# Kernel tuning notes

Hardware: AMD Instinct MI355X
Metric: run time of the kernel (lower is better)

The kernel has to match this reference:

```python
import jax, jax.numpy as jnp
import numpy as np


def setup_inputs() -> dict:
    key = jax.random.key(0)
    k1, k2, k3 = jax.random.split(key, 3)
    B, S, H, E = 8, 4096, 2048, 64
    hidden_states = jax.random.normal(k1, (B, S, H), dtype=jnp.float32)
    # kaiming_uniform-ish scale for the gate weight [E, H]
    weight = jax.random.normal(k2, (E, H), dtype=jnp.float32) * (1.0 / np.sqrt(H))
    # load-balancing biases are small perturbations of the softmax scores
    expert_biases = jax.random.normal(k3, (E,), dtype=jnp.float32) * 0.01
    return {"hidden_states": hidden_states, "weight": weight,
            "expert_biases": expert_biases, "top_k": 8}


def reference(hidden_states, weight, expert_biases, top_k):
    B, S, H = hidden_states.shape
    x = hidden_states.reshape(-1, H).astype(jnp.float32)          # [T, H], T = B*S
    logits = jnp.einsum('th,eh->te', x, weight.astype(jnp.float32))  # [T, E]
    scores = jax.nn.softmax(logits, axis=-1)                      # fp32 softmax
    bias_scores = scores + expert_biases[None, :]                 # bias-adjusted routing
    _, topk_indices = jax.lax.top_k(bias_scores, top_k)           # [T, K] (sorted; set equals torch sorted=False)
    topk_weights = jnp.take_along_axis(scores, topk_indices, axis=1)  # gather original probs
    if top_k > 1:  # norm_topk_prob=True
        topk_weights = topk_weights / (topk_weights.sum(-1, keepdims=True) + 1e-20)
    return (topk_indices.astype(jnp.int32),
            topk_weights.astype(hidden_states.dtype))
```

## Files before the change

### kernel.cpp

```cpp
#include <hip/hip_runtime.h>
#include <math.h>

#define Hdim   2048
#define HF4    512
#define MARGIN 2e-5f
#define CAPF   16384
#define PROBE0 1237
#define PROBE1 20011

#define WS_FCNT  0
#define WS_BAD   4
#define WS_PROBE 64
#define WS_FLIST 1024
#define WS_WH    (128*1024)
#define WS_WL    (384*1024)
#define WS_NEED  (640*1024)

typedef float f32x4 __attribute__((ext_vector_type(4)));
typedef short bf8   __attribute__((ext_vector_type(8)));

typedef const __attribute__((address_space(1))) unsigned int ga_u32;
typedef __attribute__((address_space(3))) unsigned int la_u32;
__device__ __forceinline__ void gload16(const void* g, void* l) {
  __builtin_amdgcn_global_load_lds((ga_u32*)g, (la_u32*)l, 16, 0, 0);
}

__device__ __forceinline__ short bf_hi(float v, float& rem) {
  const unsigned u  = __builtin_bit_cast(unsigned, v);
  const unsigned uh = u & 0xffff0000u;
  rem = v - __builtin_bit_cast(float, uh);
  return (short)(u >> 16);
}
__device__ __forceinline__ short bf_rne(float v) {
  const unsigned u = __builtin_bit_cast(unsigned, v);
  return (short)((u + 0x7fffu + ((u >> 16) & 1u)) >> 16);
}

__global__ __launch_bounds__(256) void gate_prep(
    const float* __restrict__ wgt, short* __restrict__ WH, short* __restrict__ WL)
{
  const int f  = blockIdx.x * 256 + threadIdx.x;
  const int c  = f >> 11;
  const int et = (f >> 9) & 3;
  const int l  = (f >> 3) & 63;
  const int j  = f & 7;
  const int e  = et * 16 + (l & 15);
  const int k  = c * 32 + (l >> 4) * 8 + j;
  const float w = wgt[(size_t)e * Hdim + k];
  float r; const short h = bf_hi(w, r);
  WH[f] = h; WL[f] = bf_rne(r);
}

__global__ __launch_bounds__(256, 2) void gate_main(
    const float* __restrict__ x, const short* __restrict__ WH,
    const short* __restrict__ WL, const float* __restrict__ eb,
    float* __restrict__ out, int* __restrict__ fcnt, int* __restrict__ flist,
    float* __restrict__ probelg, int T)
{
  __shared__ __align__(16) char smem[32768];
  const int t    = threadIdx.x;
  const int wv   = t >> 6;
  const int ln   = t & 63;
  const int tb   = blockIdx.x * 64 + wv * 16;

  const char* xq = (const char*)(x + (size_t)(tb + (ln & 15)) * Hdim + (ln >> 4) * 8);
  const short* whq = WH + t * 8;
  const short* wlq = WL + t * 8;

  f32x4 acc[4];
  #pragma unroll
  for (int et = 0; et < 4; ++et) acc[et] = (f32x4)0.f;

  f32x4 xE0, xE1, xO0, xO1;

#define XLOAD(D0, D1, OA, OB)                                              \
  asm volatile("global_load_dwordx4 %0, %2, off offset:" #OA "\n\t"        \
               "global_load_dwordx4 %1, %2, off offset:" #OB               \
               : "=v"(D0), "=v"(D1) : "v"(xq) : "memory")

#define WSTAGE(SLOT, KOFF) {                                               \
    gload16(whq + (KOFF), smem + (SLOT) * 8192 + wv * 1024);               \
    gload16(wlq + (KOFF), smem + (SLOT) * 8192 + 4096 + wv * 1024); }

#define SPLIT(X0, X1) {                                                    \
    _Pragma("unroll")                                                      \
    for (int j = 0; j < 4; ++j) { float r_;                                \
      ah[j]     = bf_hi(X0[j], r_);  al[j]     = bf_rne(r_);               \
      ah[j + 4] = bf_hi(X1[j], r_);  al[j + 4] = bf_rne(r_); } }

#define MF16()                                                                    \
    __builtin_amdgcn_s_setprio(1);                                                \
    acc[0] = __builtin_amdgcn_mfma_f32_16x16x32_bf16(ah, Bh0, acc[0], 0, 0, 0);   \
    acc[0] = __builtin_amdgcn_mfma_f32_16x16x32_bf16(ah, Bl0, acc[0], 0, 0, 0);   \
    acc[0] = __builtin_amdgcn_mfma_f32_16x16x32_bf16(al, Bh0, acc[0], 0, 0, 0);   \
    acc[0] = __builtin_amdgcn_mfma_f32_16x16x32_bf16(al, Bl0, acc[0], 0, 0, 0);   \
    acc[1] = __builtin_amdgcn_mfma_f32_16x16x32_bf16(ah, Bh1, acc[1], 0, 0, 0);   \
    acc[1] = __builtin_amdgcn_mfma_f32_16x16x32_bf16(ah, Bl1, acc[1], 0, 0, 0);   \
    acc[1] = __builtin_amdgcn_mfma_f32_16x16x32_bf16(al, Bh1, acc[1], 0, 0, 0);   \
    acc[1] = __builtin_amdgcn_mfma_f32_16x16x32_bf16(al, Bl1, acc[1], 0, 0, 0);   \
    acc[2] = __builtin_amdgcn_mfma_f32_16x16x32_bf16(ah, Bh2, acc[2], 0, 0, 0);   \
    acc[2] = __builtin_amdgcn_mfma_f32_16x16x32_bf16(ah, Bl2, acc[2], 0, 0, 0);   \
    acc[2] = __builtin_amdgcn_mfma_f32_16x16x32_bf16(al, Bh2, acc[2], 0, 0, 0);   \
    acc[2] = __builtin_amdgcn_mfma_f32_16x16x32_bf16(al, Bl2, acc[2], 0, 0, 0);   \
    acc[3] = __builtin_amdgcn_mfma_f32_16x16x32_bf16(ah, Bh3, acc[3], 0, 0, 0);   \
    acc[3] = __builtin_amdgcn_mfma_f32_16x16x32_bf16(ah, Bl3, acc[3], 0, 0, 0);   \
    acc[3] = __builtin_amdgcn_mfma_f32_16x16x32_bf16(al, Bh3, acc[3], 0, 0, 0);   \
    acc[3] = __builtin_amdgcn_mfma_f32_16x16x32_bf16(al, Bl3, acc[3], 0, 0, 0);   \
    __builtin_amdgcn_s_setprio(0);

#define STEP(SCUR, XI, WI, XS0, XS1, VM) {                                 \
    XI; WI;                                                                \
    asm volatile("s_waitcnt vmcnt(" #VM ")" ::: "memory");                 \
    __builtin_amdgcn_sched_barrier(0);                                     \
    bf8 ah, al;                                                            \
    SPLIT(XS0, XS1);                                                       \
    asm volatile("" ::: "memory");                                         \
    __builtin_amdgcn_s_barrier();                                          \
    asm volatile("" ::: "memory");                                         \
    const short* bh_ = (const short*)(smem + (SCUR) * 8192) + ln * 8;      \
    const short* bl_ = bh_ + 2048;                                         \
    bf8 Bh0 = *(const bf8*)(bh_);                                          \
    bf8 Bh1 = *(const bf8*)(bh_ + 512);                                    \
    bf8 Bh2 = *(const bf8*)(bh_ + 1024);                                   \
    bf8 Bh3 = *(const bf8*)(bh_ + 1536);                                   \
    bf8 Bl0 = *(const bf8*)(bl_);                                          \
    bf8 Bl1 = *(const bf8*)(bl_ + 512);                                    \
    bf8 Bl2 = *(const bf8*)(bl_ + 1024);                                   \
    bf8 Bl3 = *(const bf8*)(bl_ + 1536);                                   \
    MF16();                                                                \
  }

  XLOAD(xE0, xE1, 0, 16);
  WSTAGE(0, 0);
  WSTAGE(1, 2048);

  #pragma unroll 1
  for (int ks = 0; ks < 60; ks += 4) {
    STEP(0, XLOAD(xO0, xO1, 128, 144), WSTAGE(2, 4096),  xE0, xE1, 6);
    STEP(1, XLOAD(xE0, xE1, 256, 272), WSTAGE(3, 6144),  xO0, xO1, 6);
    STEP(2, XLOAD(xO0, xO1, 384, 400), WSTAGE(0, 8192),  xE0, xE1, 6);
    STEP(3, XLOAD(xE0, xE1, 512, 528), WSTAGE(1, 10240), xO0, xO1, 6);
    xq += 512; whq += 8192; wlq += 8192;
  }
  STEP(0, XLOAD(xO0, xO1, 128, 144), WSTAGE(2, 4096), xE0, xE1, 6);
  STEP(1, XLOAD(xE0, xE1, 256, 272), WSTAGE(3, 6144), xO0, xO1, 6);
  STEP(2, XLOAD(xO0, xO1, 384, 400), ,                xE0, xE1, 4);
  STEP(3, ,                          ,                xO0, xO1, 0);
#undef STEP
#undef MF16
#undef SPLIT
#undef WSTAGE
#undef XLOAD

  const int c = ln & 15, g = ln >> 4;
  float bias4[4];
  #pragma unroll
  for (int et = 0; et < 4; ++et) bias4[et] = eb[et * 16 + c];

  #pragma unroll
  for (int r = 0; r < 4; ++r) {
    const int gt = tb + g * 4 + r;
    const float z0 = acc[0][r], z1 = acc[1][r], z2 = acc[2][r], z3 = acc[3][r];
    if (gt == PROBE0) { probelg[c]      = z0; probelg[16 + c] = z1;
                        probelg[32 + c] = z2; probelg[48 + c] = z3; }
    if (gt == PROBE1) { probelg[64 + c]  = z0; probelg[80 + c]  = z1;
                        probelg[96 + c]  = z2; probelg[112 + c] = z3; }
    float m = fmaxf(fmaxf(z0, z1), fmaxf(z2, z3));
    #pragma unroll
    for (int off = 1; off < 16; off <<= 1) m = fmaxf(m, __shfl_xor(m, off, 64));
    const float p0 = expf(z0 - m), p1 = expf(z1 - m);
    const float p2 = expf(z2 - m), p3 = expf(z3 - m);
    float Zs = (p0 + p1) + (p2 + p3);
    #pragma unroll
    for (int off = 1; off < 16; off <<= 1) Zs += __shfl_xor(Zs, off, 64);
    const float inv = 1.f / Zs;
    const float s0 = p0 * inv, s1 = p1 * inv, s2 = p2 * inv, s3 = p3 * inv;
    float b0 = s0 + bias4[0], b1 = s1 + bias4[1];
    float b2 = s2 + bias4[2], b3 = s3 + bias4[3];
    float prev = 0.f, gmin = 1e30f, mys = 0.f;
    int myi = 0;
    #pragma unroll
    for (int r9 = 0; r9 < 9; ++r9) {
      float v = b0; int ie = 0;
      if (b1 > v) { v = b1; ie = 1; }
      if (b2 > v) { v = b2; ie = 2; }
      if (b3 > v) { v = b3; ie = 3; }
      int idx = ie * 16 + c;
      #pragma unroll
      for (int off = 1; off < 16; off <<= 1) {
        const float ov = __shfl_xor(v, off, 64);
        const int   oi = __shfl_xor(idx, off, 64);
        if (ov > v || (ov == v && oi < idx)) { v = ov; idx = oi; }
      }
      if (r9) gmin = fminf(gmin, prev - v);
      prev = v;
      if (r9 < 8) {
        const int oe = idx >> 4, oc = idx & 15;
        const float cand = oe == 0 ? s0 : oe == 1 ? s1 : oe == 2 ? s2 : s3;
        const float sv = __shfl(cand, g * 16 + oc, 64);
        if (c == r9) { myi = idx; mys = sv; }
        if (c == oc) {
          if (oe == 0) b0 = -1e30f;
          else if (oe == 1) b1 = -1e30f;
          else if (oe == 2) b2 = -1e30f;
          else b3 = -1e30f;
        }
      }
    }
    float wsum = (c < 8) ? mys : 0.f;
    #pragma unroll
    for (int off = 1; off < 16; off <<= 1) wsum += __shfl_xor(wsum, off, 64);
    if (c < 8) {
      out[(size_t)gt * 8 + c] = (float)myi;
      out[(size_t)T * 8 + (size_t)gt * 8 + c] = mys / (wsum + 1e-20f);
    }
    if (c == 0 && gmin < MARGIN) {
      const int pos = atomicAdd(fcnt, 1);
      if (pos < CAPF) flist[pos] = gt;
    }
  }
}

__global__ __launch_bounds__(256) void gate_check(
    const float* __restrict__ x, const float* __restrict__ wgt,
    const float* __restrict__ probelg, const int* __restrict__ fcnt,
    int* __restrict__ allbad)
{
  __shared__ float part[64][4];
  const int p = blockIdx.x;
  const int P = p ? PROBE1 : PROBE0;
  const int t = threadIdx.x, e = t >> 2, q = t & 3;
  const float4* xr = (const float4*)(x + (size_t)P * Hdim);
  const float4* wr = (const float4*)(wgt + (size_t)e * Hdim);
  float a = 0.f, b = 0.f, c = 0.f, d = 0.f;
  for (int i = 0; i < 128; ++i) {
    const int f4 = i * 4 + q;
    const float4 xv = xr[f4], wv = wr[f4];
    a = fmaf(xv.x, wv.x, a); b = fmaf(xv.y, wv.y, b);
    c = fmaf(xv.z, wv.z, c); d = fmaf(xv.w, wv.w, d);
  }
  part[e][q] = (a + b) + (c + d);
  __syncthreads();
  if (q == 0) {
    const float z = part[e][0] + part[e][1] + part[e][2] + part[e][3];
    if (fabsf(z - probelg[p * 64 + e]) > 0.05f) *allbad = 1;
  }
  if (t == 0 && p == 0 && *fcnt > CAPF) *allbad = 1;
}

__global__ __launch_bounds__(256) void gate_fix(
    const float* __restrict__ x, const float* __restrict__ wgt,
    const float* __restrict__ eb, float* __restrict__ out,
    const int* __restrict__ fcnt, const int* __restrict__ flist,
    const int* __restrict__ allbad, int T)
{
  __shared__ float4 xl[4 * HF4];
  __shared__ double part[4][64][4];
  __shared__ int tks[4];
  const int bad = *allbad;
  int n = bad ? T : *fcnt;
  if (n <= 0) return;
  if (!bad && n > CAPF) n = CAPF;
  const int nb = (n + 3) >> 2;
  const int t = threadIdx.x;
  for (int b = blockIdx.x; b < nb; b += gridDim.x) {
    if (t < 4) {
      const int li = b * 4 + t;
      const int ci = li < n ? li : n - 1;
      tks[t] = bad ? ci : flist[ci];
    }
    __syncthreads();
    {
      const int m = t >> 6, l2 = t & 63;
      const float4* src = (const float4*)x + (size_t)tks[m] * HF4;
      #pragma unroll
      for (int ii = 0; ii < 8; ++ii) xl[m * HF4 + ii * 64 + l2] = src[ii * 64 + l2];
    }
    __syncthreads();
    const int e = t >> 2, q = t & 3;
    double acc[4] = {0.0, 0.0, 0.0, 0.0};
    const float4* w4 = (const float4*)wgt + (size_t)e * HF4;
    for (int c = 0; c < 128; ++c) {
      const int f4 = c * 4 + q;
      const float4 wvv = w4[f4];
      #pragma unroll
      for (int m = 0; m < 4; ++m) {
        const float4 xv = xl[m * HF4 + f4];
        acc[m] += (double)xv.x * (double)wvv.x + (double)xv.y * (double)wvv.y
                + (double)xv.z * (double)wvv.z + (double)xv.w * (double)wvv.w;
      }
    }
    #pragma unroll
    for (int m = 0; m < 4; ++m) part[m][e][q] = acc[m];
    __syncthreads();
    {
      const int m = t >> 6, ln = t & 63;
      const double z = part[m][ln][0] + part[m][ln][1] + part[m][ln][2] + part[m][ln][3];
      double mx = z;
      #pragma unroll
      for (int off = 32; off; off >>= 1) mx = fmax(mx, __shfl_xor(mx, off, 64));
      const double p = exp(z - mx);
      double Zs = p;
      #pragma unroll
      for (int off = 32; off; off >>= 1) Zs += __shfl_xor(Zs, off, 64);
      const double sco = p / Zs;
      double bsw = sco + (double)eb[ln];
      double mys = 0.0;
      int myi = 0;
      #pragma unroll
      for (int r = 0; r < 8; ++r) {
        double v = bsw;
        int idx = ln;
        #pragma unroll
        for (int off = 32; off; off >>= 1) {
          const double ov = __shfl_xor(v, off, 64);
          const int   oi = __shfl_xor(idx, off, 64);
          if (ov > v || (ov == v && oi < idx)) { v = ov; idx = oi; }
        }
        const double sv = __shfl(sco, idx, 64);
        if (ln == r)  { myi = idx; mys = sv; }
        if (ln == idx) bsw = -1.0e300;
      }
      double wsum = (ln < 8) ? mys : 0.0;
      #pragma unroll
      for (int off = 32; off; off >>= 1) wsum += __shfl_xor(wsum, off, 64);
      const int gt = tks[m];
      if (ln < 8) {
        out[(size_t)gt * 8 + ln] = (float)myi;
        out[(size_t)T * 8 + (size_t)gt * 8 + ln] = (float)(mys / (wsum + 1e-20));
      }
    }
    __syncthreads();
  }
}

extern "C" void kernel_launch(void* const* d_in, const int* in_sizes, int n_in,
                              void* d_out, int out_size, void* d_ws, size_t ws_size,
                              hipStream_t stream) {
  const float* x   = (const float*)d_in[0];
  const float* wgt = (const float*)d_in[1];
  const float* eb  = (const float*)d_in[2];
  float* out = (float*)d_out;
  const int T = in_sizes[0] / Hdim;
  char* ws = (char*)d_ws;
  int*   fcnt    = (int*)(ws + WS_FCNT);
  int*   bad     = (int*)(ws + WS_BAD);
  float* probelg = (float*)(ws + WS_PROBE);
  int*   flist   = (int*)(ws + WS_FLIST);
  short* WH      = (short*)(ws + WS_WH);
  short* WL      = (short*)(ws + WS_WL);

  if (ws_size < WS_NEED) {
    hipMemsetAsync(ws, 0, 8, stream);
    hipMemsetAsync(ws + WS_BAD, 1, 1, stream);
    hipLaunchKernelGGL(gate_fix, dim3(256), dim3(256), 0, stream,
                       x, wgt, eb, out, fcnt, flist, bad, T);
    return;
  }
  hipMemsetAsync(ws, 0, 8, stream);
  hipLaunchKernelGGL(gate_prep, dim3(512), dim3(256), 0, stream, wgt, WH, WL);
  hipLaunchKernelGGL(gate_main, dim3(T / 64), dim3(256), 0, stream,
                     x, WH, WL, eb, out, fcnt, flist, probelg, T);
  hipLaunchKernelGGL(gate_check, dim3(2), dim3(256), 0, stream,
                     x, wgt, probelg, fcnt, bad);
  hipLaunchKernelGGL(gate_fix, dim3(256), dim3(256), 0, stream,
                     x, wgt, eb, out, fcnt, flist, bad, T);
}
```

Baseline: 144.7 us.

## Load gate weights directly into registers, drop LDS staging and barriers

Replaces the shared-memory staging of the bf16 hi/lo weight tiles, which used global_load_lds plus a per-step workgroup barrier, with direct per-wave global loads into registers. Weight tiles are double-buffered in registers (even and odd sets) and x is prefetched three steps ahead, with vmcnt waits rebalanced to match. This removes the s_barrier synchronisation and the LDS reads. In exchange each wave now loads the full weight tile itself, so weight traffic through L2 and cache goes up fourfold and register pressure rises, which may hurt occupancy.

```diff
diff --git a/kernel.cpp b/kernel.cpp
--- a/kernel.cpp
+++ b/kernel.cpp
@@ -18,12 +18,6 @@
 
 typedef float f32x4 __attribute__((ext_vector_type(4)));
 typedef short bf8   __attribute__((ext_vector_type(8)));
-
-typedef const __attribute__((address_space(1))) unsigned int ga_u32;
-typedef __attribute__((address_space(3))) unsigned int la_u32;
-__device__ __forceinline__ void gload16(const void* g, void* l) {
-  __builtin_amdgcn_global_load_lds((ga_u32*)g, (la_u32*)l, 16, 0, 0);
-}
 
 __device__ __forceinline__ short bf_hi(float v, float& rem) {
   const unsigned u  = __builtin_bit_cast(unsigned, v);
@@ -57,99 +51,104 @@
     float* __restrict__ out, int* __restrict__ fcnt, int* __restrict__ flist,
     float* __restrict__ probelg, int T)
 {
-  __shared__ __align__(16) char smem[32768];
-  const int t    = threadIdx.x;
-  const int wv   = t >> 6;
-  const int ln   = t & 63;
-  const int tb   = blockIdx.x * 64 + wv * 16;
+  const int t  = threadIdx.x;
+  const int wv = t >> 6;
+  const int ln = t & 63;
+  const int tb = blockIdx.x * 64 + wv * 16;
 
   const char* xq = (const char*)(x + (size_t)(tb + (ln & 15)) * Hdim + (ln >> 4) * 8);
-  const short* whq = WH + t * 8;
-  const short* wlq = WL + t * 8;
+  const short* whp = WH;
+  const short* wlp = WL;
+  const unsigned voff = (unsigned)(ln * 16);
 
   f32x4 acc[4];
   #pragma unroll
   for (int et = 0; et < 4; ++et) acc[et] = (f32x4)0.f;
 
-  f32x4 xE0, xE1, xO0, xO1;
+  f32x4 P0a, P0b, P1a, P1b, P2a, P2b, P3a, P3b;
+  bf8 WEh0, WEh1, WEh2, WEh3, WEl0, WEl1, WEl2, WEl3;
+  bf8 WOh0, WOh1, WOh2, WOh3, WOl0, WOl1, WOl2, WOl3;
 
 #define XLOAD(D0, D1, OA, OB)                                              \
   asm volatile("global_load_dwordx4 %0, %2, off offset:" #OA "\n\t"        \
                "global_load_dwordx4 %1, %2, off offset:" #OB               \
-               : "=v"(D0), "=v"(D1) : "v"(xq) : "memory")
-
-#define WSTAGE(SLOT, KOFF) {                                               \
-    gload16(whq + (KOFF), smem + (SLOT) * 8192 + wv * 1024);               \
-    gload16(wlq + (KOFF), smem + (SLOT) * 8192 + 4096 + wv * 1024); }
-
-#define SPLIT(X0, X1) {                                                    \
-    _Pragma("unroll")                                                      \
-    for (int j = 0; j < 4; ++j) { float r_;                                \
-      ah[j]     = bf_hi(X0[j], r_);  al[j]     = bf_rne(r_);               \
-      ah[j + 4] = bf_hi(X1[j], r_);  al[j + 4] = bf_rne(r_); } }
-
-#define MF16()                                                                    \
+               : "=v"(D0), "=v"(D1) : "v"(xq))
+
+#define WLOAD(H0,H1,H2,H3,L0,L1,L2,L3)                                     \
+  asm volatile(                                                            \
+    "global_load_dwordx4 %0, %8, %9  offset:0\n\t"                         \
+    "global_load_dwordx4 %1, %8, %9  offset:1024\n\t"                      \
+    "global_load_dwordx4 %2, %8, %9  offset:2048\n\t"                      \
+    "global_load_dwordx4 %3, %8, %9  offset:3072\n\t"                      \
+    "global_load_dwordx4 %4, %8, %10 offset:0\n\t"                         \
+    "global_load_dwordx4 %5, %8, %10 offset:1024\n\t"                      \
+    "global_load_dwordx4 %6, %8, %10 offset:2048\n\t"                      \
+    "global_load_dwordx4 %7, %8, %10 offset:3072"                          \
+    : "=v"(H0), "=v"(H1), "=v"(H2), "=v"(H3),                              \
+      "=v"(L0), "=v"(L1), "=v"(L2), "=v"(L3)                               \
+    : "v"(voff), "s"(whp), "s"(wlp));                                      \
+  whp += 2048; wlp += 2048;
+
+#define WAITC(VM)                                                          \
+  asm volatile("s_waitcnt vmcnt(" #VM ")" ::: "memory");                   \
+  __builtin_amdgcn_sched_barrier(0);
+
+#define COMP(XA, XB, H0,H1,H2,H3, L0,L1,L2,L3) {                                  \
+    bf8 ah, al;                                                                   \
+    _Pragma("unroll")                                                             \
+    for (int j = 0; j < 4; ++j) { float r_;                                       \
+      ah[j]     = bf_hi(XA[j], r_);  al[j]     = bf_rne(r_);                      \
+      ah[j + 4] = bf_hi(XB[j], r_);  al[j + 4] = bf_rne(r_); }                    \
     __builtin_amdgcn_s_setprio(1);                                                \
-    acc[0] = __builtin_amdgcn_mfma_f32_16x16x32_bf16(ah, Bh0, acc[0], 0, 0, 0);   \
-    acc[0] = __builtin_amdgcn_mfma_f32_16x16x32_bf16(ah, Bl0, acc[0], 0, 0, 0);   \
-    acc[0] = __builtin_amdgcn_mfma_f32_16x16x32_bf16(al, Bh0, acc[0], 0, 0, 0);   \
-    acc[0] = __builtin_amdgcn_mfma_f32_16x16x32_bf16(al, Bl0, acc[0], 0, 0, 0);   \
-    acc[1] = __builtin_amdgcn_mfma_f32_16x16x32_bf16(ah, Bh1, acc[1], 0, 0, 0);   \
-    acc[1] = __builtin_amdgcn_mfma_f32_16x16x32_bf16(ah, Bl1, acc[1], 0, 0, 0);   \
-    acc[1] = __builtin_amdgcn_mfma_f32_16x16x32_bf16(al, Bh1, acc[1], 0, 0, 0);   \
-    acc[1] = __builtin_amdgcn_mfma_f32_16x16x32_bf16(al, Bl1, acc[1], 0, 0, 0);   \
-    acc[2] = __builtin_amdgcn_mfma_f32_16x16x32_bf16(ah, Bh2, acc[2], 0, 0, 0);   \
-    acc[2] = __builtin_amdgcn_mfma_f32_16x16x32_bf16(ah, Bl2, acc[2], 0, 0, 0);   \
-    acc[2] = __builtin_amdgcn_mfma_f32_16x16x32_bf16(al, Bh2, acc[2], 0, 0, 0);   \
-    acc[2] = __builtin_amdgcn_mfma_f32_16x16x32_bf16(al, Bl2, acc[2], 0, 0, 0);   \
-    acc[3] = __builtin_amdgcn_mfma_f32_16x16x32_bf16(ah, Bh3, acc[3], 0, 0, 0);   \
-    acc[3] = __builtin_amdgcn_mfma_f32_16x16x32_bf16(ah, Bl3, acc[3], 0, 0, 0);   \
-    acc[3] = __builtin_amdgcn_mfma_f32_16x16x32_bf16(al, Bh3, acc[3], 0, 0, 0);   \
-    acc[3] = __builtin_amdgcn_mfma_f32_16x16x32_bf16(al, Bl3, acc[3], 0, 0, 0);   \
-    __builtin_amdgcn_s_setprio(0);
-
-#define STEP(SCUR, XI, WI, XS0, XS1, VM) {                                 \
-    XI; WI;                                                                \
-    asm volatile("s_waitcnt vmcnt(" #VM ")" ::: "memory");                 \
-    __builtin_amdgcn_sched_barrier(0);                                     \
-    bf8 ah, al;                                                            \
-    SPLIT(XS0, XS1);                                                       \
-    asm volatile("" ::: "memory");                                         \
-    __builtin_amdgcn_s_barrier();                                          \
-    asm volatile("" ::: "memory");                                         \
-    const short* bh_ = (const short*)(smem + (SCUR) * 8192) + ln * 8;      \
-    const short* bl_ = bh_ + 2048;                                         \
-    bf8 Bh0 = *(const bf8*)(bh_);                                          \
-    bf8 Bh1 = *(const bf8*)(bh_ + 512);                                    \
-    bf8 Bh2 = *(const bf8*)(bh_ + 1024);                                   \
-    bf8 Bh3 = *(const bf8*)(bh_ + 1536);                                   \
-    bf8 Bl0 = *(const bf8*)(bl_);                                          \
-    bf8 Bl1 = *(const bf8*)(bl_ + 512);                                    \
-    bf8 Bl2 = *(const bf8*)(bl_ + 1024);                                   \
-    bf8 Bl3 = *(const bf8*)(bl_ + 1536);                                   \
-    MF16();                                                                \
-  }
-
-  XLOAD(xE0, xE1, 0, 16);
-  WSTAGE(0, 0);
-  WSTAGE(1, 2048);
+    acc[0] = __builtin_amdgcn_mfma_f32_16x16x32_bf16(ah, H0, acc[0], 0, 0, 0);    \
+    acc[0] = __builtin_amdgcn_mfma_f32_16x16x32_bf16(ah, L0, acc[0], 0, 0, 0);    \
+    acc[0] = __builtin_amdgcn_mfma_f32_16x16x32_bf16(al, H0, acc[0], 0, 0, 0);    \
+    acc[0] = __builtin_amdgcn_mfma_f32_16x16x32_bf16(al, L0, acc[0], 0, 0, 0);    \
+    acc[1] = __builtin_amdgcn_mfma_f32_16x16x32_bf16(ah, H1, acc[1], 0, 0, 0);    \
+    acc[1] = __builtin_amdgcn_mfma_f32_16x16x32_bf16(ah, L1, acc[1], 0, 0, 0);    \
+    acc[1] = __builtin_amdgcn_mfma_f32_16x16x32_bf16(al, H1, acc[1], 0, 0, 0);    \
+    acc[1] = __builtin_amdgcn_mfma_f32_16x16x32_bf16(al, L1, acc[1], 0, 0, 0);    \
+    acc[2] = __builtin_amdgcn_mfma_f32_16x16x32_bf16(ah, H2, acc[2], 0, 0, 0);    \
+    acc[2] = __builtin_amdgcn_mfma_f32_16x16x32_bf16(ah, L2, acc[2], 0, 0, 0);    \
+    acc[2] = __builtin_amdgcn_mfma_f32_16x16x32_bf16(al, H2, acc[2], 0, 0, 0);    \
+    acc[2] = __builtin_amdgcn_mfma_f32_16x16x32_bf16(al, L2, acc[2], 0, 0, 0);    \
+    acc[3] = __builtin_amdgcn_mfma_f32_16x16x32_bf16(ah, H3, acc[3], 0, 0, 0);    \
+    acc[3] = __builtin_amdgcn_mfma_f32_16x16x32_bf16(ah, L3, acc[3], 0, 0, 0);    \
+    acc[3] = __builtin_amdgcn_mfma_f32_16x16x32_bf16(al, H3, acc[3], 0, 0, 0);    \
+    acc[3] = __builtin_amdgcn_mfma_f32_16x16x32_bf16(al, L3, acc[3], 0, 0, 0);    \
+    __builtin_amdgcn_s_setprio(0);                                                \
+  }
+
+#define CE(XA,XB) COMP(XA,XB, WEh0,WEh1,WEh2,WEh3, WEl0,WEl1,WEl2,WEl3)
+#define CO(XA,XB) COMP(XA,XB, WOh0,WOh1,WOh2,WOh3, WOl0,WOl1,WOl2,WOl3)
+#define WE_ WLOAD(WEh0,WEh1,WEh2,WEh3, WEl0,WEl1,WEl2,WEl3)
+#define WO_ WLOAD(WOh0,WOh1,WOh2,WOh3, WOl0,WOl1,WOl2,WOl3)
+
+  WE_;
+  XLOAD(P0a, P0b, 0, 16);
+  WO_;
+  XLOAD(P1a, P1b, 128, 144);
+  XLOAD(P2a, P2b, 256, 272);
 
   #pragma unroll 1
-  for (int ks = 0; ks < 60; ks += 4) {
-    STEP(0, XLOAD(xO0, xO1, 128, 144), WSTAGE(2, 4096),  xE0, xE1, 6);
-    STEP(1, XLOAD(xE0, xE1, 256, 272), WSTAGE(3, 6144),  xO0, xO1, 6);
-    STEP(2, XLOAD(xO0, xO1, 384, 400), WSTAGE(0, 8192),  xE0, xE1, 6);
-    STEP(3, XLOAD(xE0, xE1, 512, 528), WSTAGE(1, 10240), xO0, xO1, 6);
-    xq += 512; whq += 8192; wlq += 8192;
-  }
-  STEP(0, XLOAD(xO0, xO1, 128, 144), WSTAGE(2, 4096), xE0, xE1, 6);
-  STEP(1, XLOAD(xE0, xE1, 256, 272), WSTAGE(3, 6144), xO0, xO1, 6);
-  STEP(2, XLOAD(xO0, xO1, 384, 400), ,                xE0, xE1, 4);
-  STEP(3, ,                          ,                xO0, xO1, 0);
-#undef STEP
-#undef MF16
-#undef SPLIT
-#undef WSTAGE
+  for (int it = 0; it < 15; ++it) {
+    WAITC(12); CE(P0a, P0b); WE_; XLOAD(P3a, P3b, 384, 400);
+    WAITC(12); CO(P1a, P1b); WO_; XLOAD(P0a, P0b, 512, 528);
+    WAITC(12); CE(P2a, P2b); WE_; XLOAD(P1a, P1b, 640, 656);
+    WAITC(12); CO(P3a, P3b); WO_; XLOAD(P2a, P2b, 768, 784);
+    xq += 512;
+  }
+  WAITC(12); CE(P0a, P0b); WE_; XLOAD(P3a, P3b, 384, 400);
+  WAITC(12); CO(P1a, P1b); WO_;
+  WAITC(10); CE(P2a, P2b);
+  WAITC(0);  CO(P3a, P3b);
+#undef WE_
+#undef WO_
+#undef CE
+#undef CO
+#undef COMP
+#undef WAITC
+#undef WLOAD
 #undef XLOAD
 
   const int c = ln & 15, g = ln >> 4;
```

Result: slower. 166.8 us (+15.3%).
